# Kernel optimization log

Hardware: AMD Instinct MI355X
Metric: run time of the kernel (lower is better)

The kernel has to match this reference:

```python
import jax, jax.numpy as jnp
import numpy as np

D_MODEL = 1024
NUM_HEADS = 16
DEPTH = D_MODEL // NUM_HEADS


def setup_inputs() -> dict:
    key = jax.random.key(0)
    ks = jax.random.split(key, 11)
    B, S, D = 2, 2048, D_MODEL
    s = 1.0 / np.sqrt(D)
    inp = {
        'x': jax.random.normal(ks[0], (B, S, D), jnp.float32),
        'pH': jax.random.normal(ks[1], (B, 1, 1), jnp.float32),
        'Wq': jax.random.normal(ks[2], (D, D), jnp.float32) * s,
        'bq': jnp.zeros((D,), jnp.float32),
        'Wk': jax.random.normal(ks[3], (D, D), jnp.float32) * s,
        'bk': jnp.zeros((D,), jnp.float32),
        'Wv': jax.random.normal(ks[4], (D, D), jnp.float32) * s,
        'bv': jnp.zeros((D,), jnp.float32),
        'Wo': jax.random.normal(ks[5], (D, D), jnp.float32) * s,
        'bo': jnp.zeros((D,), jnp.float32),
    }
    return inp


def reference(x, pH, Wq, bq, Wk, bk, Wv, bv, Wo, bo):
    B, S, D = x.shape
    H, dh = NUM_HEADS, DEPTH
    # QKV projections -> [B, H, S, dh]
    def proj(W, b):
        return (x @ W + b).reshape(B, S, H, dh).transpose(0, 2, 1, 3)
    q = proj(Wq, bq)
    k = proj(Wk, bk)
    v = proj(Wv, bv)
    # scores [B, H, S, S] with additive per-sample pH bias broadcast over heads/positions
    scores = jnp.einsum('bhqd,bhkd->bhqk', q, k) / jnp.sqrt(jnp.asarray(dh, x.dtype))
    scores = scores + pH[:, :, :, None]  # [B,1,1,1] broadcasts to [B,H,S,S]
    attn = jax.nn.softmax(scores, axis=-1)
    out = jnp.einsum('bhqk,bhkd->bhqd', attn, v)  # [B,H,S,dh]
    out = out.transpose(0, 2, 1, 3).reshape(B, S, D)
    return out @ Wo + bo  # dropout p=0.0 -> identity
```

## Files before the change

### kernel.cpp

```cpp
#include <hip/hip_runtime.h>
#include <hip/hip_bf16.h>
#include <math.h>

#define BATCH 2
#define SEQ   2048
#define DMODEL 1024
#define NHEADS 16
#define DHEAD 64
#define MROWS (BATCH*SEQ)

typedef __attribute__((ext_vector_type(8))) short bf16x8;
typedef __attribute__((ext_vector_type(4))) short bf16x4;
typedef __attribute__((ext_vector_type(4))) float f32x4;

__device__ __forceinline__ short f2bf(float f) {
    union { float f; unsigned u; } c; c.f = f;
    unsigned r = (c.u + 0x7fffu + ((c.u >> 16) & 1u)) >> 16;
    return (short)r;
}

__device__ __forceinline__ void async_ld16(const void* g, void* l) {
    __builtin_amdgcn_global_load_lds(
        (const __attribute__((address_space(1))) unsigned*)g,
        (__attribute__((address_space(3))) unsigned*)l, 16, 0, 0);
}

__global__ __launch_bounds__(256) void prep(
    const float* __restrict__ x, short* __restrict__ xhi,
    const float* __restrict__ W0, const float* __restrict__ W1,
    const float* __restrict__ W2, const float* __restrict__ W3,
    short* __restrict__ oqkv, short* __restrict__ oo)
{
    __shared__ float T[64][65];
    const int tid = threadIdx.x;
    if (blockIdx.x < 2048) {
        const int i = blockIdx.x * 256 + tid;
        const float4* p = (const float4*)x + (size_t)i * 2;
        float4 a = p[0], b = p[1];
        float v[8] = {a.x, a.y, a.z, a.w, b.x, b.y, b.z, b.w};
        bf16x8 H;
        #pragma unroll
        for (int j = 0; j < 8; ++j) H[j] = f2bf(v[j]);
        *((bf16x8*)xhi + i) = H;
        return;
    }
    const int bi = blockIdx.x - 2048;
    const int z = bi >> 8;
    const int t = bi & 255;
    const float* W = (z == 0) ? W0 : (z == 1) ? W1 : (z == 2) ? W2 : W3;
    short* out = (z < 3) ? (oqkv + (size_t)z * 1024 * 1024) : oo;
    const int n0 = (t & 15) * 64, k0 = (t >> 4) * 64;
    #pragma unroll
    for (int i = 0; i < 16; ++i) {
        const int idx = tid + i * 256;
        const int r = idx >> 6, c = idx & 63;
        T[r][c] = W[(size_t)(k0 + r) * DMODEL + n0 + c];
    }
    __syncthreads();
    #pragma unroll
    for (int i = 0; i < 4; ++i) {
        const int idx = tid + i * 256;
        const int r = idx >> 4, g = idx & 15;
        bf16x4 H;
        #pragma unroll
        for (int j = 0; j < 4; ++j)
            H[j] = f2bf(T[g * 4 + j][r]);
        *(bf16x4*)(out + (size_t)(n0 + r) * DMODEL + k0 + g * 4) = H;
    }
}

#define GBK 64

__global__ __launch_bounds__(256) void mfma_gemm(
    const short* __restrict__ Ahi, const short* __restrict__ Bthi,
    const float* __restrict__ b0, const float* __restrict__ b1, const float* __restrict__ b2,
    short* __restrict__ oqh, short* __restrict__ okh, short* __restrict__ ovh,
    float* __restrict__ outf, int mode, float qscale)
{
    __shared__ short Ah[128 * GBK], Bh[128 * GBK];

    const int tid  = threadIdx.x;
    const int lane = tid & 63;
    const int w    = tid >> 6;
    const int quad = lane >> 4;
    const int l15  = lane & 15;
    const int wr   = w >> 1, wc = w & 1;
    const int m0   = blockIdx.y * 128;
    const int n0   = blockIdx.x * 128;
    const int K    = DMODEL;

    f32x4 acc[4][4] = {};

    int srow[4], spos[4];
    #pragma unroll
    for (int j = 0; j < 4; ++j) {
        const int c = w * 256 + j * 64 + lane;
        srow[j] = c >> 3;
        spos[j] = (c & 7) ^ (srow[j] & 7);
    }

    for (int k0 = 0; k0 < K; k0 += GBK) {
        __syncthreads();
        #pragma unroll
        for (int j = 0; j < 4; ++j) {
            const int cB = (w * 256 + j * 64) * 8;
            async_ld16(Ahi + (size_t)(m0 + srow[j]) * K + k0 + spos[j] * 8, Ah + cB);
            async_ld16(Bthi + (size_t)(n0 + srow[j]) * K + k0 + spos[j] * 8, Bh + cB);
        }
        __syncthreads();

        #pragma unroll
        for (int s = 0; s < 2; ++s) {
            bf16x8 afh[4], bfh[4];
            #pragma unroll
            for (int mi = 0; mi < 4; ++mi) {
                const int row = wr * 64 + mi * 16 + l15;
                const int pos = (s * 4 + quad) ^ (row & 7);
                afh[mi] = *(const bf16x8*)(Ah + row * GBK + pos * 8);
            }
            #pragma unroll
            for (int ni = 0; ni < 4; ++ni) {
                const int row = wc * 64 + ni * 16 + l15;
                const int pos = (s * 4 + quad) ^ (row & 7);
                bfh[ni] = *(const bf16x8*)(Bh + row * GBK + pos * 8);
            }
            #pragma unroll
            for (int mi = 0; mi < 4; ++mi)
                #pragma unroll
                for (int ni = 0; ni < 4; ++ni)
                    acc[mi][ni] = __builtin_amdgcn_mfma_f32_16x16x32_bf16(
                        afh[mi], bfh[ni], acc[mi][ni], 0, 0, 0);
        }
    }

    const int nbase = n0 + wc * 64;
    if (mode == 1) {
        #pragma unroll
        for (int mi = 0; mi < 4; ++mi)
            #pragma unroll
            for (int ni = 0; ni < 4; ++ni)
                #pragma unroll
                for (int r = 0; r < 4; ++r) {
                    const int m = m0 + wr * 64 + mi * 16 + quad * 4 + r;
                    const int nn = nbase + ni * 16 + l15;
                    outf[(size_t)m * DMODEL + nn] = acc[mi][ni][r] + b0[nn];
                }
    } else {
        __syncthreads();
        short* scr = (w < 2) ? (Ah + w * 4096) : (Bh + (w - 2) * 4096);
        const int which = nbase >> 10;
        const int hh = (nbase & 1023) >> 6;
        const int mb = m0 + wr * 64;
        const int b = mb >> 11, sbase = mb & (SEQ - 1);

        if (which < 2) {
            const float* bias = which ? b1 : b0;
            short* dstp = which ? okh : oqh;
            const float scl = which ? 1.0f : qscale;
            #pragma unroll
            for (int mi = 0; mi < 4; ++mi)
                #pragma unroll
                for (int ni = 0; ni < 4; ++ni)
                    #pragma unroll
                    for (int r = 0; r < 4; ++r) {
                        const int sloc = mi * 16 + quad * 4 + r;
                        const int dloc = ni * 16 + l15;
                        const int nn = (nbase + ni * 16 + l15) & 1023;
                        scr[sloc * 64 + (((dloc >> 3) ^ (sloc & 7)) * 8) + (dloc & 7)] =
                            f2bf((acc[mi][ni][r] + bias[nn]) * scl);
                    }
            #pragma unroll
            for (int i = 0; i < 8; ++i) {
                const int sloc = i * 8 + (lane >> 3);
                const int cph = (lane & 7) ^ (sloc & 7);
                bf16x8 row = *(const bf16x8*)(scr + sloc * 64 + cph * 8);
                const int dloc = (lane & 7) * 8;
                *(bf16x8*)(dstp + ((size_t)(b * NHEADS + hh) * SEQ + sbase + sloc) * DHEAD + dloc) = row;
            }
        } else {
            #pragma unroll
            for (int mi = 0; mi < 4; ++mi)
                #pragma unroll
                for (int ni = 0; ni < 4; ++ni)
                    #pragma unroll
                    for (int r = 0; r < 4; ++r) {
                        const int sloc = mi * 16 + quad * 4 + r;
                        const int dloc = ni * 16 + l15;
                        const int nn = (nbase + ni * 16 + l15) & 1023;
                        scr[dloc * 64 + (((sloc >> 3) ^ (dloc & 7)) * 8) + (sloc & 7)] =
                            f2bf(acc[mi][ni][r] + b2[nn]);
                    }
            #pragma unroll
            for (int i = 0; i < 8; ++i) {
                const int dloc = i * 8 + (lane >> 3);
                const int cph = (lane & 7) ^ (dloc & 7);
                bf16x8 row = *(const bf16x8*)(scr + dloc * 64 + cph * 8);
                const int sg = sbase + (lane & 7) * 8;
                *(bf16x8*)(ovh + ((size_t)(b * NHEADS + hh) * DHEAD + dloc) * SEQ + sg) = row;
            }
        }
    }
}

#define PP 72

__global__ __launch_bounds__(256) void attn_mfma(
    const short* __restrict__ Qh_g, const short* __restrict__ Kh_g,
    const short* __restrict__ Vth_g,
    float* __restrict__ op0, float* __restrict__ op1,
    float* __restrict__ l0g, float* __restrict__ l1g)
{
    __shared__ short Ksh[2][4096];
    __shared__ short Vsh[2][4096];
    __shared__ short Ph[4][2][16 * PP];

    const int tid  = threadIdx.x;
    const int lane = tid & 63;
    const int w    = tid >> 6;
    const int quad = lane >> 4;
    const int l15  = lane & 15;

    const int bh    = blockIdx.x & 31;
    const int sk    = (blockIdx.x >> 5) & 1;
    const int qtile = blockIdx.x >> 6;
    const int q0    = qtile * 128 + w * 32;
    const size_t kvb = (size_t)bh * SEQ * DHEAD;

    bf16x8 ones;
    #pragma unroll
    for (int j = 0; j < 8; ++j) ones[j] = (short)0x3f80;

    bf16x8 qA[2], qB[2];
    {
        const size_t qrA = kvb + (size_t)(q0 + l15) * DHEAD;
        const size_t qrB = kvb + (size_t)(q0 + 16 + l15) * DHEAD;
        qA[0] = *(const bf16x8*)(Qh_g + qrA + quad * 8);
        qA[1] = *(const bf16x8*)(Qh_g + qrA + 32 + quad * 8);
        qB[0] = *(const bf16x8*)(Qh_g + qrB + quad * 8);
        qB[1] = *(const bf16x8*)(Qh_g + qrB + 32 + quad * 8);
    }

    const bool isv = (w >= 2);
    int srow[4], spos[4];
    #pragma unroll
    for (int j = 0; j < 4; ++j) {
        const int c = (w & 1) * 256 + j * 64 + lane;
        srow[j] = c >> 3;
        spos[j] = (c & 7) ^ (srow[j] & 7);
    }

    auto stage = [&](int buf, int kb) {
        short* d = isv ? Vsh[buf] : Ksh[buf];
        const short* src = isv ? (Vth_g + kvb + kb) : (Kh_g + kvb + (size_t)kb * DHEAD);
        #pragma unroll
        for (int j = 0; j < 4; ++j) {
            const short* g = src + (isv ? ((size_t)srow[j] * SEQ + spos[j] * 8)
                                        : ((size_t)srow[j] * DHEAD + spos[j] * 8));
            async_ld16(g, d + ((w & 1) * 256 + j * 64) * 8);
        }
    };

    f32x4 oA[4] = {}, oB[4] = {};
    f32x4 lAv = {}, lBv = {};

    const int kb0 = sk * (SEQ / 2), kb1 = kb0 + SEQ / 2;
    stage(0, kb0);
    int pb = 0;
    for (int kb = kb0; kb < kb1; kb += 64, pb ^= 1) {
        __syncthreads();
        if (kb + 64 < kb1) stage(pb ^ 1, kb + 64);

        const short* Kb = Ksh[pb];
        const short* Vb = Vsh[pb];

        #pragma unroll
        for (int mf = 0; mf < 4; ++mf) {
            const int row = mf * 16 + l15;
            const int sw = row & 7;
            bf16x8 kh0 = *(const bf16x8*)(Kb + row * 64 + ((quad ^ sw) * 8));
            bf16x8 kh1 = *(const bf16x8*)(Kb + row * 64 + (((4 + quad) ^ sw) * 8));
            f32x4 cA = {}, cB = {};
            cA = __builtin_amdgcn_mfma_f32_16x16x32_bf16(kh0, qA[0], cA, 0, 0, 0);
            cA = __builtin_amdgcn_mfma_f32_16x16x32_bf16(kh1, qA[1], cA, 0, 0, 0);
            cB = __builtin_amdgcn_mfma_f32_16x16x32_bf16(kh0, qB[0], cB, 0, 0, 0);
            cB = __builtin_amdgcn_mfma_f32_16x16x32_bf16(kh1, qB[1], cB, 0, 0, 0);

            unsigned uA[4], uB[4];
            #pragma unroll
            for (int r = 0; r < 4; ++r) {
                union { float f; unsigned u; } p;
                p.f = __builtin_amdgcn_exp2f(cA[r]);
                uA[r] = p.u;
                p.f = __builtin_amdgcn_exp2f(cB[r]);
                uB[r] = p.u;
            }
            uint2 pkA, pkB;
            pkA.x = __builtin_amdgcn_perm(uA[1], uA[0], 0x07060302u);
            pkA.y = __builtin_amdgcn_perm(uA[3], uA[2], 0x07060302u);
            pkB.x = __builtin_amdgcn_perm(uB[1], uB[0], 0x07060302u);
            pkB.y = __builtin_amdgcn_perm(uB[3], uB[2], 0x07060302u);
            *(uint2*)(&Ph[w][0][l15 * PP + mf * 16 + quad * 4]) = pkA;
            *(uint2*)(&Ph[w][1][l15 * PP + mf * 16 + quad * 4]) = pkB;
        }

        bf16x8 pA0 = *(const bf16x8*)(&Ph[w][0][l15 * PP + quad * 8]);
        bf16x8 pA1 = *(const bf16x8*)(&Ph[w][0][l15 * PP + 32 + quad * 8]);
        bf16x8 pB0 = *(const bf16x8*)(&Ph[w][1][l15 * PP + quad * 8]);
        bf16x8 pB1 = *(const bf16x8*)(&Ph[w][1][l15 * PP + 32 + quad * 8]);

        lAv = __builtin_amdgcn_mfma_f32_16x16x32_bf16(pA0, ones, lAv, 0, 0, 0);
        lAv = __builtin_amdgcn_mfma_f32_16x16x32_bf16(pA1, ones, lAv, 0, 0, 0);
        lBv = __builtin_amdgcn_mfma_f32_16x16x32_bf16(pB0, ones, lBv, 0, 0, 0);
        lBv = __builtin_amdgcn_mfma_f32_16x16x32_bf16(pB1, ones, lBv, 0, 0, 0);

        #pragma unroll
        for (int nf = 0; nf < 4; ++nf) {
            const int row = nf * 16 + l15;
            const int sw = row & 7;
            bf16x8 vh0 = *(const bf16x8*)(Vb + row * 64 + ((quad ^ sw) * 8));
            bf16x8 vh1 = *(const bf16x8*)(Vb + row * 64 + (((4 + quad) ^ sw) * 8));
            f32x4 cA = oA[nf], cB = oB[nf];
            cA = __builtin_amdgcn_mfma_f32_16x16x32_bf16(pA0, vh0, cA, 0, 0, 0);
            cA = __builtin_amdgcn_mfma_f32_16x16x32_bf16(pA1, vh1, cA, 0, 0, 0);
            cB = __builtin_amdgcn_mfma_f32_16x16x32_bf16(pB0, vh0, cB, 0, 0, 0);
            cB = __builtin_amdgcn_mfma_f32_16x16x32_bf16(pB1, vh1, cB, 0, 0, 0);
            oA[nf] = cA; oB[nf] = cB;
        }
    }

    float* op = sk ? op1 : op0;
    float* lg = sk ? l1g : l0g;
    const int b = bh >> 4, hh = bh & 15;
    #pragma unroll
    for (int r = 0; r < 4; ++r) {
        const int qa = q0 + quad * 4 + r;
        if (l15 == 0) {
            lg[bh * SEQ + qa] = lAv[r];
            lg[bh * SEQ + qa + 16] = lBv[r];
        }
    }
    #pragma unroll
    for (int nf = 0; nf < 4; ++nf) {
        #pragma unroll
        for (int r = 0; r < 4; ++r) {
            const int qa = q0 + quad * 4 + r;
            const int d = nf * 16 + l15;
            op[(size_t)(b * SEQ + qa) * DMODEL + hh * DHEAD + d] = oA[nf][r];
            op[(size_t)(b * SEQ + qa + 16) * DMODEL + hh * DHEAD + d] = oB[nf][r];
        }
    }
}

__global__ __launch_bounds__(256) void combine_o(
    const float* __restrict__ op0, const float* __restrict__ op1,
    const float* __restrict__ l0g, const float* __restrict__ l1g,
    short* __restrict__ aoh)
{
    const int i = blockIdx.x * 256 + threadIdx.x;
    const size_t e = (size_t)i * 8;
    const int qg = (int)(e >> 10);
    const int col = (int)(e & 1023);
    const int b = qg >> 11;
    const int q = qg & (SEQ - 1);
    const int bh = b * NHEADS + (col >> 6);
    const float inv = 1.0f / (l0g[bh * SEQ + q] + l1g[bh * SEQ + q]);

    float4 a0 = *(const float4*)(op0 + e);
    float4 a1 = *(const float4*)(op0 + e + 4);
    float4 c0 = *(const float4*)(op1 + e);
    float4 c1 = *(const float4*)(op1 + e + 4);
    bf16x8 H;
    H[0] = f2bf((a0.x + c0.x) * inv);
    H[1] = f2bf((a0.y + c0.y) * inv);
    H[2] = f2bf((a0.z + c0.z) * inv);
    H[3] = f2bf((a0.w + c0.w) * inv);
    H[4] = f2bf((a1.x + c1.x) * inv);
    H[5] = f2bf((a1.y + c1.y) * inv);
    H[6] = f2bf((a1.z + c1.z) * inv);
    H[7] = f2bf((a1.w + c1.w) * inv);
    *((bf16x8*)aoh + i) = H;
}

extern "C" void kernel_launch(void* const* d_in, const int* in_sizes, int n_in,
                              void* d_out, int out_size, void* d_ws, size_t ws_size,
                              hipStream_t stream) {
    const float* x  = (const float*)d_in[0];
    const float* Wq = (const float*)d_in[2];
    const float* bq = (const float*)d_in[3];
    const float* Wk = (const float*)d_in[4];
    const float* bk = (const float*)d_in[5];
    const float* Wv = (const float*)d_in[6];
    const float* bv = (const float*)d_in[7];
    const float* Wo = (const float*)d_in[8];
    const float* bo = (const float*)d_in[9];
    float* out = (float*)d_out;

    char* ws = (char*)d_ws;
    const size_t MB = 1024 * 1024;
    short* qh  = (short*)(ws + 0 * MB);
    short* kh  = (short*)(ws + 16 * MB);
    short* vth = (short*)(ws + 32 * MB);
    short* aoh = (short*)(ws + 48 * MB);
    float* op0 = (float*)(ws + 56 * MB);
    short* xhi = (short*)(ws + 64 * MB);
    float* op1 = (float*)(ws + 72 * MB);
    short* wqkv_hi = (short*)(ws + 80 * MB);
    float* l0g = (float*)(ws + 88 * MB);
    float* l1g = (float*)(ws + 89 * MB);
    short* wto_hi  = (short*)(ws + 92 * MB);

    dim3 blk(256);

    hipLaunchKernelGGL(prep, dim3(2048 + 1024), blk, 0, stream,
                       x, xhi, Wq, Wk, Wv, Wo, wqkv_hi, wto_hi);

    const float qscale = 0.125f * 1.44269504088896f;
    hipLaunchKernelGGL(mfma_gemm, dim3(3072 / 128, MROWS / 128), blk, 0, stream,
                       xhi, wqkv_hi, bq, bk, bv,
                       qh, kh, vth, (float*)nullptr, 0, qscale);

    hipLaunchKernelGGL(attn_mfma, dim3(BATCH * NHEADS * (SEQ / 128) * 2), blk, 0, stream,
                       qh, kh, vth, op0, op1, l0g, l1g);

    hipLaunchKernelGGL(combine_o, dim3(MROWS * DMODEL / 8 / 256), blk, 0, stream,
                       op0, op1, l0g, l1g, aoh);

    hipLaunchKernelGGL(mfma_gemm, dim3(1024 / 128, MROWS / 128), blk, 0, stream,
                       aoh, wto_hi, bo, bo, bo,
                       (short*)nullptr, (short*)nullptr, (short*)nullptr,
                       out, 1, 1.0f);
}
```

Baseline: 213.9 us.

## Single-buffer K/V staging, swizzle P scratch, store partial outputs as bf16

The attention kernel drops double-buffered K/V LDS staging in favour of a single buffer loaded between two barriers. This halves LDS use and may raise occupancy, but global loads no longer overlap compute. The P scratch changes from a padded layout to an XOR-swizzled 64-wide layout to avoid bank conflicts. Partial attention outputs are now written as bf16 instead of fp32, halving traffic to and from the combine kernel at some precision cost.

```diff
diff --git a/kernel.cpp b/kernel.cpp
--- a/kernel.cpp
+++ b/kernel.cpp
@@ -17,6 +17,10 @@
     union { float f; unsigned u; } c; c.f = f;
     unsigned r = (c.u + 0x7fffu + ((c.u >> 16) & 1u)) >> 16;
     return (short)r;
+}
+__device__ __forceinline__ float bf2f(short h) {
+    union { unsigned u; float f; } c; c.u = ((unsigned)(unsigned short)h) << 16;
+    return c.f;
 }
 
 __device__ __forceinline__ void async_ld16(const void* g, void* l) {
@@ -202,17 +206,15 @@
     }
 }
 
-#define PP 72
-
 __global__ __launch_bounds__(256) void attn_mfma(
     const short* __restrict__ Qh_g, const short* __restrict__ Kh_g,
     const short* __restrict__ Vth_g,
-    float* __restrict__ op0, float* __restrict__ op1,
+    short* __restrict__ op0, short* __restrict__ op1,
     float* __restrict__ l0g, float* __restrict__ l1g)
 {
-    __shared__ short Ksh[2][4096];
-    __shared__ short Vsh[2][4096];
-    __shared__ short Ph[4][2][16 * PP];
+    __shared__ short Ksh[4096];
+    __shared__ short Vsh[4096];
+    __shared__ short Ph[4][2][1024];
 
     const int tid  = threadIdx.x;
     const int lane = tid & 63;
@@ -241,6 +243,7 @@
     }
 
     const bool isv = (w >= 2);
+    short* dst = isv ? Vsh : Ksh;
     int srow[4], spos[4];
     #pragma unroll
     for (int j = 0; j < 4; ++j) {
@@ -249,36 +252,29 @@
         spos[j] = (c & 7) ^ (srow[j] & 7);
     }
 
-    auto stage = [&](int buf, int kb) {
-        short* d = isv ? Vsh[buf] : Ksh[buf];
-        const short* src = isv ? (Vth_g + kvb + kb) : (Kh_g + kvb + (size_t)kb * DHEAD);
-        #pragma unroll
-        for (int j = 0; j < 4; ++j) {
-            const short* g = src + (isv ? ((size_t)srow[j] * SEQ + spos[j] * 8)
-                                        : ((size_t)srow[j] * DHEAD + spos[j] * 8));
-            async_ld16(g, d + ((w & 1) * 256 + j * 64) * 8);
-        }
-    };
-
     f32x4 oA[4] = {}, oB[4] = {};
     f32x4 lAv = {}, lBv = {};
 
     const int kb0 = sk * (SEQ / 2), kb1 = kb0 + SEQ / 2;
-    stage(0, kb0);
-    int pb = 0;
-    for (int kb = kb0; kb < kb1; kb += 64, pb ^= 1) {
+    for (int kb = kb0; kb < kb1; kb += 64) {
         __syncthreads();
-        if (kb + 64 < kb1) stage(pb ^ 1, kb + 64);
-
-        const short* Kb = Ksh[pb];
-        const short* Vb = Vsh[pb];
+        {
+            const short* src = isv ? (Vth_g + kvb + kb) : (Kh_g + kvb + (size_t)kb * DHEAD);
+            #pragma unroll
+            for (int j = 0; j < 4; ++j) {
+                const short* g = src + (isv ? ((size_t)srow[j] * SEQ + spos[j] * 8)
+                                            : ((size_t)srow[j] * DHEAD + spos[j] * 8));
+                async_ld16(g, dst + ((w & 1) * 256 + j * 64) * 8);
+            }
+        }
+        __syncthreads();
 
         #pragma unroll
         for (int mf = 0; mf < 4; ++mf) {
             const int row = mf * 16 + l15;
             const int sw = row & 7;
-            bf16x8 kh0 = *(const bf16x8*)(Kb + row * 64 + ((quad ^ sw) * 8));
-            bf16x8 kh1 = *(const bf16x8*)(Kb + row * 64 + (((4 + quad) ^ sw) * 8));
+            bf16x8 kh0 = *(const bf16x8*)(Ksh + row * 64 + ((quad ^ sw) * 8));
+            bf16x8 kh1 = *(const bf16x8*)(Ksh + row * 64 + (((4 + quad) ^ sw) * 8));
             f32x4 cA = {}, cB = {};
             cA = __builtin_amdgcn_mfma_f32_16x16x32_bf16(kh0, qA[0], cA, 0, 0, 0);
             cA = __builtin_amdgcn_mfma_f32_16x16x32_bf16(kh1, qA[1], cA, 0, 0, 0);
@@ -299,14 +295,17 @@
             pkA.y = __builtin_amdgcn_perm(uA[3], uA[2], 0x07060302u);
             pkB.x = __builtin_amdgcn_perm(uB[1], uB[0], 0x07060302u);
             pkB.y = __builtin_amdgcn_perm(uB[3], uB[2], 0x07060302u);
-            *(uint2*)(&Ph[w][0][l15 * PP + mf * 16 + quad * 4]) = pkA;
-            *(uint2*)(&Ph[w][1][l15 * PP + mf * 16 + quad * 4]) = pkB;
-        }
-
-        bf16x8 pA0 = *(const bf16x8*)(&Ph[w][0][l15 * PP + quad * 8]);
-        bf16x8 pA1 = *(const bf16x8*)(&Ph[w][0][l15 * PP + 32 + quad * 8]);
-        bf16x8 pB0 = *(const bf16x8*)(&Ph[w][1][l15 * PP + quad * 8]);
-        bf16x8 pB1 = *(const bf16x8*)(&Ph[w][1][l15 * PP + 32 + quad * 8]);
+            const int pc = (mf * 2 + (quad >> 1)) ^ (l15 & 7);
+            const int paddr = l15 * 64 + pc * 8 + (quad & 1) * 4;
+            *(uint2*)(&Ph[w][0][paddr]) = pkA;
+            *(uint2*)(&Ph[w][1][paddr]) = pkB;
+        }
+
+        const int psw = l15 & 7;
+        bf16x8 pA0 = *(const bf16x8*)(&Ph[w][0][l15 * 64 + ((quad ^ psw) * 8)]);
+        bf16x8 pA1 = *(const bf16x8*)(&Ph[w][0][l15 * 64 + (((4 + quad) ^ psw) * 8)]);
+        bf16x8 pB0 = *(const bf16x8*)(&Ph[w][1][l15 * 64 + ((quad ^ psw) * 8)]);
+        bf16x8 pB1 = *(const bf16x8*)(&Ph[w][1][l15 * 64 + (((4 + quad) ^ psw) * 8)]);
 
         lAv = __builtin_amdgcn_mfma_f32_16x16x32_bf16(pA0, ones, lAv, 0, 0, 0);
         lAv = __builtin_amdgcn_mfma_f32_16x16x32_bf16(pA1, ones, lAv, 0, 0, 0);
@@ -317,8 +316,8 @@
         for (int nf = 0; nf < 4; ++nf) {
             const int row = nf * 16 + l15;
             const int sw = row & 7;
-            bf16x8 vh0 = *(const bf16x8*)(Vb + row * 64 + ((quad ^ sw) * 8));
-            bf16x8 vh1 = *(const bf16x8*)(Vb + row * 64 + (((4 + quad) ^ sw) * 8));
+            bf16x8 vh0 = *(const bf16x8*)(Vsh + row * 64 + ((quad ^ sw) * 8));
+            bf16x8 vh1 = *(const bf16x8*)(Vsh + row * 64 + (((4 + quad) ^ sw) * 8));
             f32x4 cA = oA[nf], cB = oB[nf];
             cA = __builtin_amdgcn_mfma_f32_16x16x32_bf16(pA0, vh0, cA, 0, 0, 0);
             cA = __builtin_amdgcn_mfma_f32_16x16x32_bf16(pA1, vh1, cA, 0, 0, 0);
@@ -328,7 +327,7 @@
         }
     }
 
-    float* op = sk ? op1 : op0;
+    short* op = sk ? op1 : op0;
     float* lg = sk ? l1g : l0g;
     const int b = bh >> 4, hh = bh & 15;
     #pragma unroll
@@ -345,14 +344,14 @@
         for (int r = 0; r < 4; ++r) {
             const int qa = q0 + quad * 4 + r;
             const int d = nf * 16 + l15;
-            op[(size_t)(b * SEQ + qa) * DMODEL + hh * DHEAD + d] = oA[nf][r];
-            op[(size_t)(b * SEQ + qa + 16) * DMODEL + hh * DHEAD + d] = oB[nf][r];
+            op[(size_t)(b * SEQ + qa) * DMODEL + hh * DHEAD + d] = f2bf(oA[nf][r]);
+            op[(size_t)(b * SEQ + qa + 16) * DMODEL + hh * DHEAD + d] = f2bf(oB[nf][r]);
         }
     }
 }
 
 __global__ __launch_bounds__(256) void combine_o(
-    const float* __restrict__ op0, const float* __restrict__ op1,
+    const short* __restrict__ op0, const short* __restrict__ op1,
     const float* __restrict__ l0g, const float* __restrict__ l1g,
     short* __restrict__ aoh)
 {
@@ -365,19 +364,12 @@
     const int bh = b * NHEADS + (col >> 6);
     const float inv = 1.0f / (l0g[bh * SEQ + q] + l1g[bh * SEQ + q]);
 
-    float4 a0 = *(const float4*)(op0 + e);
-    float4 a1 = *(const float4*)(op0 + e + 4);
-    float4 c0 = *(const float4*)(op1 + e);
-    float4 c1 = *(const float4*)(op1 + e + 4);
+    bf16x8 a = *((const bf16x8*)op0 + i);
+    bf16x8 c = *((const bf16x8*)op1 + i);
     bf16x8 H;
-    H[0] = f2bf((a0.x + c0.x) * inv);
-    H[1] = f2bf((a0.y + c0.y) * inv);
-    H[2] = f2bf((a0.z + c0.z) * inv);
-    H[3] = f2bf((a0.w + c0.w) * inv);
-    H[4] = f2bf((a1.x + c1.x) * inv);
-    H[5] = f2bf((a1.y + c1.y) * inv);
-    H[6] = f2bf((a1.z + c1.z) * inv);
-    H[7] = f2bf((a1.w + c1.w) * inv);
+    #pragma unroll
+    for (int j = 0; j < 8; ++j)
+        H[j] = f2bf((bf2f(a[j]) + bf2f(c[j])) * inv);
     *((bf16x8*)aoh + i) = H;
 }
 
@@ -401,9 +393,9 @@
     short* kh  = (short*)(ws + 16 * MB);
     short* vth = (short*)(ws + 32 * MB);
     short* aoh = (short*)(ws + 48 * MB);
-    float* op0 = (float*)(ws + 56 * MB);
+    short* op0 = (short*)(ws + 56 * MB);
     short* xhi = (short*)(ws + 64 * MB);
-    float* op1 = (float*)(ws + 72 * MB);
+    short* op1 = (short*)(ws + 72 * MB);
     short* wqkv_hi = (short*)(ws + 80 * MB);
     float* l0g = (float*)(ws + 88 * MB);
     float* l1g = (float*)(ws + 89 * MB);
```

Result: faster. 205.9 us (-3.8%).
